# Optimization experiments

Hardware: AMD Instinct MI355X
Metric: run time of the kernel (lower is better)

Reference implementation:

```python
import jax, jax.numpy as jnp
import numpy as np

NUM_GRAPHS = 64

def setup_inputs() -> dict:
    key = jax.random.key(0)
    ks = jax.random.split(key, 10)
    N, E, D, V = 100000, 1600000, 64, 30
    node_types = jax.random.randint(ks[0], (N,), 0, V, dtype=jnp.int64 if jax.config.jax_enable_x64 else jnp.int32)
    edge_index = jax.random.randint(ks[1], (2, E), 0, N, dtype=jnp.int32)
    batch = jnp.sort(jax.random.randint(ks[2], (N,), 0, NUM_GRAPHS, dtype=jnp.int32))
    emb_table = jax.random.normal(ks[3], (V, D), dtype=jnp.float32)
    W1 = jax.random.normal(ks[4], (D, D), dtype=jnp.float32) / np.sqrt(D)
    W2 = jax.random.normal(ks[5], (D, D), dtype=jnp.float32) / np.sqrt(D)
    W3 = jax.random.normal(ks[6], (D, D), dtype=jnp.float32) / np.sqrt(D)
    b1 = jnp.zeros((D,), jnp.float32)
    b2 = jnp.zeros((D,), jnp.float32)
    b3 = jnp.zeros((D,), jnp.float32)
    return {"node_types": node_types, "edge_index": edge_index, "batch": batch,
            "emb_table": emb_table, "W1": W1, "b1": b1, "W2": W2, "b2": b2, "W3": W3, "b3": b3}

def _gcn_conv(x, W, b, row, col, norm, N):
    # x' = D^-1/2 (A+I) D^-1/2 (x @ W) + b   (PyG GCNConv semantics)
    h = x @ W
    msg = h[row] * norm[:, None]              # gather + edgewise scale
    out = jax.ops.segment_sum(msg, col, num_segments=N)  # scatter-add at targets
    return out + b

def reference(node_types, edge_index, batch, emb_table, W1, b1, W2, b2, W3, b3):
    N = node_types.shape[0]
    # add self-loops
    loops = jnp.arange(N, dtype=edge_index.dtype)
    row = jnp.concatenate([edge_index[0], loops])
    col = jnp.concatenate([edge_index[1], loops])
    # symmetric normalization on A + I
    deg = jax.ops.segment_sum(jnp.ones_like(col, dtype=jnp.float32), col, num_segments=N)
    dinv = jnp.where(deg > 0, jax.lax.rsqrt(deg), 0.0)
    norm = dinv[row] * dinv[col]
    x = emb_table[node_types]
    x = jax.nn.relu(_gcn_conv(x, W1, b1, row, col, norm, N))
    x = jax.nn.relu(_gcn_conv(x, W2, b2, row, col, norm, N))
    x = _gcn_conv(x, W3, b3, row, col, norm, N)
    # global mean pool over batch segments
    sums = jax.ops.segment_sum(x, batch, num_segments=NUM_GRAPHS)
    cnts = jax.ops.segment_sum(jnp.ones((N,), jnp.float32), batch, num_segments=NUM_GRAPHS)
    pooled = sums / jnp.maximum(cnts, 1.0)[:, None]
    # L2 normalize rows
    return pooled / jnp.linalg.norm(pooled, axis=1, keepdims=True)
```

## Files before the change

### kernel.cpp

```cpp
#include <hip/hip_runtime.h>
#include <hip/hip_fp16.h>

#define DD 64
#define NUM_GRAPHS 64
#define AGG_BLOCKS 2048
#define EB 512
#define BINW 256
#define MAXNB 512
#define EBIN_CAP 6144

typedef _Float16 h2_t __attribute__((ext_vector_type(2)));

__device__ __forceinline__ float fdot2u(unsigned a, unsigned b, float c) {
    return __builtin_amdgcn_fdot2(__builtin_bit_cast(h2_t, a),
                                  __builtin_bit_cast(h2_t, b), c, false);
}

__global__ __launch_bounds__(256) void k_hist(const int* __restrict__ col,
                                              int* __restrict__ H, int E, int NB, int CE) {
    __shared__ int h[MAXNB];
    int eb = blockIdx.x, t = threadIdx.x;
    for (int i = t; i < NB; i += 256) h[i] = 0;
    __syncthreads();
    int e0 = eb * CE, e1 = min(E, e0 + CE);
    for (int e = e0 + t; e < e1; e += 256) atomicAdd(&h[col[e] >> 8], 1);
    __syncthreads();
    for (int i = t; i < NB; i += 256) H[eb * NB + i] = h[i];
}

__global__ __launch_bounds__(256) void k_scanA(int* __restrict__ H,
                                               int* __restrict__ bintot, int NB) {
    __shared__ int s[256];
    int b = blockIdx.x, t = threadIdx.x;
    int i0 = (2 * t) * NB + b, i1 = (2 * t + 1) * NB + b;
    int v0 = H[i0], v1 = H[i1];
    int tot = v0 + v1;
    s[t] = tot;
    __syncthreads();
    for (int off = 1; off < 256; off <<= 1) {
        int tv = (t >= off) ? s[t - off] : 0;
        __syncthreads();
        s[t] += tv;
        __syncthreads();
    }
    int excl = s[t] - tot;
    H[i0] = excl;
    H[i1] = excl + v0;
    if (t == 255) bintot[b] = s[255];
}

__global__ void k_scanB(const int* __restrict__ bintot, int* __restrict__ binstart, int NB) {
    __shared__ int s[512];
    int t = threadIdx.x;
    int v = (t < NB) ? bintot[t] : 0;
    s[t] = v;
    __syncthreads();
    for (int off = 1; off < 512; off <<= 1) {
        int tv = (t >= off) ? s[t - off] : 0;
        __syncthreads();
        s[t] += tv;
        __syncthreads();
    }
    if (t < NB) binstart[t] = s[t] - v;
    if (t == 511) binstart[NB] = s[511];
}

__global__ __launch_bounds__(256) void k_scatbin(const int* __restrict__ row,
                                                 const int* __restrict__ col,
                                                 const int* __restrict__ H,
                                                 const int* __restrict__ binstart,
                                                 unsigned* __restrict__ binned,
                                                 int E, int NB, int CE) {
    __shared__ int off[MAXNB];
    int eb = blockIdx.x, t = threadIdx.x;
    for (int i = t; i < NB; i += 256) off[i] = binstart[i] + H[eb * NB + i];
    __syncthreads();
    int e0 = eb * CE, e1 = min(E, e0 + CE);
    for (int e = e0 + t; e < e1; e += 256) {
        int c = col[e], r = row[e];
        int slot = atomicAdd(&off[c >> 8], 1);
        binned[slot] = ((unsigned)(c & 255) << 24) | (unsigned)r;
    }
}

__global__ __launch_bounds__(256) void k_bincsr(const unsigned* __restrict__ binned,
                                                const int* __restrict__ binstart,
                                                const int* __restrict__ nt,
                                                int* __restrict__ srcidx,
                                                int* __restrict__ rowptr,
                                                float* __restrict__ dinv,
                                                int2* __restrict__ pk, int N, int NB) {
    __shared__ unsigned arr[EBIN_CAP];
    __shared__ int sorted_[EBIN_CAP];
    __shared__ int cnt[BINW];
    __shared__ int base[BINW];
    __shared__ int cursor[BINW];
    int b = blockIdx.x, t = threadIdx.x;
    int s0 = binstart[b], s1 = binstart[b + 1];
    int binsz = s1 - s0;
    if (binsz > EBIN_CAP) binsz = EBIN_CAP;
    cnt[t] = 0;
    for (int i = t; i < binsz; i += 256) arr[i] = binned[s0 + i];
    __syncthreads();
    for (int i = t; i < binsz; i += 256) atomicAdd(&cnt[arr[i] >> 24], 1);
    __syncthreads();
    int v = cnt[t];
    base[t] = v;
    __syncthreads();
    for (int off = 1; off < 256; off <<= 1) {
        int tv = (t >= off) ? base[t - off] : 0;
        __syncthreads();
        base[t] += tv;
        __syncthreads();
    }
    int excl = base[t] - v;
    __syncthreads();
    base[t] = excl;
    cursor[t] = excl;
    __syncthreads();
    for (int i = t; i < binsz; i += 256) {
        unsigned val = arr[i];
        int pos = atomicAdd(&cursor[val >> 24], 1);
        sorted_[pos] = (int)(val & 0xFFFFFF);
    }
    __syncthreads();
    for (int i = t; i < binsz; i += 256) srcidx[s0 + i] = sorted_[i];
    int node = b * BINW + t;
    if (node < N) {
        rowptr[node] = s0 + base[t];
        float di = rsqrtf((float)cnt[t] + 1.0f);
        dinv[node] = di;
        pk[node] = make_int2(nt[node], __float_as_int(di));
    }
    if (b == NB - 1 && t == 0) rowptr[N] = s1;
}

__global__ void k_buildepk(const int* __restrict__ srcidx, const int2* __restrict__ pk,
                           unsigned* __restrict__ epku, int E) {
    int i = blockIdx.x * blockDim.x + threadIdx.x;
    if (i >= E) return;
    int2 p = pk[srcidx[i]];
    epku[i] = ((unsigned)p.x << 16) |
              (unsigned)__half_as_ushort(__float2half(__int_as_float(p.y)));
}

__global__ void k_embW1(const float* __restrict__ emb, const float* __restrict__ W1,
                        float* __restrict__ embW1, int V) {
    __shared__ float er[DD];
    int v = blockIdx.x, j = threadIdx.x;
    er[j] = emb[v * DD + j];
    __syncthreads();
    float acc = 0.0f;
    #pragma unroll
    for (int d = 0; d < DD; ++d) acc += er[d] * W1[d * DD + j];
    embW1[v * DD + j] = acc;
}

__global__ void k_packW(const float* __restrict__ W, unsigned* __restrict__ Wpk) {
    int t = blockIdx.x * blockDim.x + threadIdx.x;
    if (t >= 32 * DD) return;
    int p = t >> 6, j = t & 63;
    __half2 h = __floats2half2_rn(W[(2 * p) * DD + j], W[(2 * p + 1) * DD + j]);
    Wpk[t] = __builtin_bit_cast(unsigned, h);
}

__device__ __forceinline__ float epi_dot_full(float v, const unsigned* Wc) {
    float vn = __shfl_xor(v, 1, 64);
    __half2 pr = __floats2half2_rn(v, vn);
    int vpk = __builtin_bit_cast(int, pr);
    float o0 = 0.f, o1 = 0.f, o2 = 0.f, o3 = 0.f;
    #pragma unroll
    for (int p = 0; p < 32; p += 4) {
        o0 = fdot2u((unsigned)__builtin_amdgcn_readlane(vpk, 2 * (p + 0)), Wc[p + 0], o0);
        o1 = fdot2u((unsigned)__builtin_amdgcn_readlane(vpk, 2 * (p + 1)), Wc[p + 1], o1);
        o2 = fdot2u((unsigned)__builtin_amdgcn_readlane(vpk, 2 * (p + 2)), Wc[p + 2], o2);
        o3 = fdot2u((unsigned)__builtin_amdgcn_readlane(vpk, 2 * (p + 3)), Wc[p + 3], o3);
    }
    return (o0 + o1) + (o2 + o3);
}

__device__ __forceinline__ float epi_dot_q(float4 v, const unsigned* Wc) {
    __half2 h0 = __floats2half2_rn(v.x, v.y);
    __half2 h1 = __floats2half2_rn(v.z, v.w);
    int vp0 = __builtin_bit_cast(int, h0);
    int vp1 = __builtin_bit_cast(int, h1);
    float o0 = 0.f, o1 = 0.f, o2 = 0.f, o3 = 0.f;
    #pragma unroll
    for (int p = 0; p < 32; p += 4) {
        o0 = fdot2u((unsigned)__builtin_amdgcn_readlane(vp0, (p + 0) >> 1), Wc[p + 0], o0);
        o1 = fdot2u((unsigned)__builtin_amdgcn_readlane(vp1, (p + 1) >> 1), Wc[p + 1], o1);
        o2 = fdot2u((unsigned)__builtin_amdgcn_readlane(vp0, (p + 2) >> 1), Wc[p + 2], o2);
        o3 = fdot2u((unsigned)__builtin_amdgcn_readlane(vp1, (p + 3) >> 1), Wc[p + 3], o3);
    }
    return (o0 + o1) + (o2 + o3);
}

__device__ __forceinline__ void acc_h4(float4& a, uint2 r) {
    float2 f0 = __half22float2(*(const __half2*)&r.x);
    float2 f1 = __half22float2(*(const __half2*)&r.y);
    a.x += f0.x; a.y += f0.y; a.z += f1.x; a.w += f1.y;
}

__device__ __forceinline__ float4 gather_sum_q(const int* __restrict__ srcidx,
                                               const __half* __restrict__ Hs,
                                               int s, int e, int g, int l) {
    float4 A = {0,0,0,0}, B = {0,0,0,0}, C = {0,0,0,0}, D = {0,0,0,0};
    int k = s;
    int kend = s + ((e - s) & ~15);
    if (k < kend) {
        uint2 r0 = *(const uint2*)(Hs + (long)srcidx[k + g] * DD + 4 * l);
        uint2 r1 = *(const uint2*)(Hs + (long)srcidx[k + 4 + g] * DD + 4 * l);
        uint2 r2 = *(const uint2*)(Hs + (long)srcidx[k + 8 + g] * DD + 4 * l);
        uint2 r3 = *(const uint2*)(Hs + (long)srcidx[k + 12 + g] * DD + 4 * l);
        k += 16;
        for (; k < kend; k += 16) {
            uint2 n0 = *(const uint2*)(Hs + (long)srcidx[k + g] * DD + 4 * l);
            uint2 n1 = *(const uint2*)(Hs + (long)srcidx[k + 4 + g] * DD + 4 * l);
            uint2 n2 = *(const uint2*)(Hs + (long)srcidx[k + 8 + g] * DD + 4 * l);
            uint2 n3 = *(const uint2*)(Hs + (long)srcidx[k + 12 + g] * DD + 4 * l);
            acc_h4(A, r0); acc_h4(B, r1); acc_h4(C, r2); acc_h4(D, r3);
            r0 = n0; r1 = n1; r2 = n2; r3 = n3;
        }
        acc_h4(A, r0); acc_h4(B, r1); acc_h4(C, r2); acc_h4(D, r3);
    }
    for (; k < e; k += 4) {
        if (k + g < e) {
            uint2 rr = *(const uint2*)(Hs + (long)srcidx[k + g] * DD + 4 * l);
            acc_h4(A, rr);
        }
    }
    A.x += B.x + C.x + D.x; A.y += B.y + C.y + D.y;
    A.z += B.z + C.z + D.z; A.w += B.w + C.w + D.w;
    A.x += __shfl_xor(A.x, 16, 64); A.x += __shfl_xor(A.x, 32, 64);
    A.y += __shfl_xor(A.y, 16, 64); A.y += __shfl_xor(A.y, 32, 64);
    A.z += __shfl_xor(A.z, 16, 64); A.z += __shfl_xor(A.z, 32, 64);
    A.w += __shfl_xor(A.w, 16, 64); A.w += __shfl_xor(A.w, 32, 64);
    return A;
}

__global__ __launch_bounds__(256, 4) void k_agg1_fused(const int* __restrict__ rowptr,
                                                    const unsigned* __restrict__ epku,
                                                    const int2* __restrict__ pk,
                                                    const float* __restrict__ embW1,
                                                    const float* __restrict__ b1,
                                                    const unsigned* __restrict__ W2pk,
                                                    __half* __restrict__ OUT, int N, int V) {
    __shared__ float ew[30 * DD];
    int tid = threadIdx.x;
    for (int k = tid; k < V * DD; k += 256) ew[k] = embW1[k];
    __syncthreads();
    int j = tid & 63;
    unsigned Wc[32];
    #pragma unroll
    for (int p = 0; p < 32; ++p) Wc[p] = W2pk[p * DD + j];
    float bj = b1[j];
    int wave0 = blockIdx.x * 4 + (tid >> 6);
    int wstride = gridDim.x * 4;
    for (int node = __builtin_amdgcn_readfirstlane(wave0); node < N;
         node += wstride) {
        int s = rowptr[node], e = rowptr[node + 1];
        float acc = 0.0f;
        int k = s;
        for (; k + 7 < e; k += 8) {
            unsigned u0 = epku[k],   u1 = epku[k+1], u2 = epku[k+2], u3 = epku[k+3];
            unsigned u4 = epku[k+4], u5 = epku[k+5], u6 = epku[k+6], u7 = epku[k+7];
            acc += ew[(u0 >> 16) * DD + j] * __half2float(__ushort_as_half((unsigned short)(u0 & 0xFFFF)))
                 + ew[(u1 >> 16) * DD + j] * __half2float(__ushort_as_half((unsigned short)(u1 & 0xFFFF)))
                 + ew[(u2 >> 16) * DD + j] * __half2float(__ushort_as_half((unsigned short)(u2 & 0xFFFF)))
                 + ew[(u3 >> 16) * DD + j] * __half2float(__ushort_as_half((unsigned short)(u3 & 0xFFFF)));
            acc += ew[(u4 >> 16) * DD + j] * __half2float(__ushort_as_half((unsigned short)(u4 & 0xFFFF)))
                 + ew[(u5 >> 16) * DD + j] * __half2float(__ushort_as_half((unsigned short)(u5 & 0xFFFF)))
                 + ew[(u6 >> 16) * DD + j] * __half2float(__ushort_as_half((unsigned short)(u6 & 0xFFFF)))
                 + ew[(u7 >> 16) * DD + j] * __half2float(__ushort_as_half((unsigned short)(u7 & 0xFFFF)));
        }
        for (; k < e; ++k) {
            unsigned u0 = epku[k];
            acc += ew[(u0 >> 16) * DD + j] * __half2float(__ushort_as_half((unsigned short)(u0 & 0xFFFF)));
        }
        int2 pc = pk[node];
        float dc = __int_as_float(pc.y);
        float v = (acc + ew[pc.x * DD + j] * dc) * dc + bj;
        v = fmaxf(v, 0.0f);
        OUT[(long)node * DD + j] = __float2half(epi_dot_full(v, Wc) * dc);
    }
}

__global__ __launch_bounds__(256, 4) void k_agg2_fused(const int* __restrict__ rowptr,
                                                    const int* __restrict__ srcidx,
                                                    const float* __restrict__ dinv,
                                                    const __half* __restrict__ Hs,
                                                    const float* __restrict__ b2,
                                                    const unsigned* __restrict__ W3pk,
                                                    __half* __restrict__ OUT, int N) {
    int tid = threadIdx.x;
    int lane = tid & 63;
    int g = lane >> 4, l = lane & 15;
    unsigned Wc[32];
    #pragma unroll
    for (int p = 0; p < 32; ++p) Wc[p] = W3pk[p * DD + lane];
    float4 bq = *(const float4*)(b2 + 4 * l);
    int wave0 = blockIdx.x * 4 + (tid >> 6);
    int wstride = gridDim.x * 4;
    for (int node = __builtin_amdgcn_readfirstlane(wave0); node < N;
         node += wstride) {
        int s = rowptr[node], e = rowptr[node + 1];
        float4 acc = gather_sum_q(srcidx, Hs, s, e, g, l);
        float dc = dinv[node];
        uint2 sr = *(const uint2*)(Hs + (long)node * DD + 4 * l);
        float2 s0 = __half22float2(*(const __half2*)&sr.x);
        float2 s1 = __half22float2(*(const __half2*)&sr.y);
        float4 v;
        v.x = fmaxf((acc.x + s0.x) * dc + bq.x, 0.f);
        v.y = fmaxf((acc.y + s0.y) * dc + bq.y, 0.f);
        v.z = fmaxf((acc.z + s1.x) * dc + bq.z, 0.f);
        v.w = fmaxf((acc.w + s1.y) * dc + bq.w, 0.f);
        OUT[(long)node * DD + lane] = __float2half(epi_dot_q(v, Wc) * dc);
    }
}

__global__ __launch_bounds__(256, 4) void k_agg3_pool(const int* __restrict__ rowptr,
                                                   const int* __restrict__ srcidx,
                                                   const float* __restrict__ dinv,
                                                   const __half* __restrict__ Hs,
                                                   const float* __restrict__ b3,
                                                   const int* __restrict__ batch,
                                                   float* __restrict__ pool,
                                                   int N, int chunk) {
    int tid = threadIdx.x;
    int lane = tid & 63;
    int g = lane >> 4, l = lane & 15;
    int w = __builtin_amdgcn_readfirstlane(blockIdx.x * 4 + (tid >> 6));
    int start = w * chunk;
    if (start >= N) return;
    int endn = min(N, start + chunk);
    float4 bq = *(const float4*)(b3 + 4 * l);
    int gcur = batch[start];
    float4 pacc = {0.f, 0.f, 0.f, 0.f};
    for (int node = start; node < endn; ++node) {
        int s = rowptr[node], e = rowptr[node + 1];
        float4 acc = gather_sum_q(srcidx, Hs, s, e, g, l);
        float dc = dinv[node];
        uint2 sr = *(const uint2*)(Hs + (long)node * DD + 4 * l);
        float2 s0 = __half22float2(*(const __half2*)&sr.x);
        float2 s1 = __half22float2(*(const __half2*)&sr.y);
        float4 v;
        v.x = (acc.x + s0.x) * dc + bq.x;
        v.y = (acc.y + s0.y) * dc + bq.y;
        v.z = (acc.z + s1.x) * dc + bq.z;
        v.w = (acc.w + s1.y) * dc + bq.w;
        int gb = batch[node];
        if (gb != gcur) {
            if (g == 0) {
                atomicAdd(&pool[gcur * DD + 4 * l + 0], pacc.x);
                atomicAdd(&pool[gcur * DD + 4 * l + 1], pacc.y);
                atomicAdd(&pool[gcur * DD + 4 * l + 2], pacc.z);
                atomicAdd(&pool[gcur * DD + 4 * l + 3], pacc.w);
            }
            gcur = gb;
            pacc = v;
        } else {
            pacc.x += v.x; pacc.y += v.y; pacc.z += v.z; pacc.w += v.w;
        }
    }
    if (g == 0) {
        atomicAdd(&pool[gcur * DD + 4 * l + 0], pacc.x);
        atomicAdd(&pool[gcur * DD + 4 * l + 1], pacc.y);
        atomicAdd(&pool[gcur * DD + 4 * l + 2], pacc.z);
        atomicAdd(&pool[gcur * DD + 4 * l + 3], pacc.w);
    }
}

__global__ void k_final(const float* __restrict__ pool, const int* __restrict__ batch,
                        float* __restrict__ out, int N) {
    int g = blockIdx.x, j = threadIdx.x;
    int lo = 0, hi = N;
    while (lo < hi) { int m = (lo + hi) >> 1; if (batch[m] < g) lo = m + 1; else hi = m; }
    int lo2 = lo; hi = N;
    while (lo2 < hi) { int m = (lo2 + hi) >> 1; if (batch[m] < g + 1) lo2 = m + 1; else hi = m; }
    float cnt = fmaxf((float)(lo2 - lo), 1.0f);
    float v = pool[g * DD + j] / cnt;
    float sq = v * v;
    #pragma unroll
    for (int off = 32; off > 0; off >>= 1) sq += __shfl_down(sq, off, 64);
    float nrm = __shfl(sq, 0, 64);
    out[g * DD + j] = v / sqrtf(nrm);
}

extern "C" void kernel_launch(void* const* d_in, const int* in_sizes, int n_in,
                              void* d_out, int out_size, void* d_ws, size_t ws_size,
                              hipStream_t stream) {
    const int*   node_types = (const int*)d_in[0];
    const int*   edge_index = (const int*)d_in[1];
    const int*   batch      = (const int*)d_in[2];
    const float* emb        = (const float*)d_in[3];
    const float* W1 = (const float*)d_in[4];
    const float* b1 = (const float*)d_in[5];
    const float* W2 = (const float*)d_in[6];
    const float* b2 = (const float*)d_in[7];
    const float* W3 = (const float*)d_in[8];
    const float* b3 = (const float*)d_in[9];
    const int N = in_sizes[0];
    const int E = in_sizes[1] / 2;
    const int V = in_sizes[3] / DD;
    const int* row = edge_index;
    const int* col = edge_index + E;
    const long ND = (long)N * DD;
    const int NB = (N + BINW - 1) / BINW;
    const int CE = (E + EB - 1) / EB;

    char* p = (char*)d_ws;
    __half*   hsA     = (__half*)p;       p += ND * sizeof(__half);
    __half*   hsB     = (__half*)p;       p += ND * sizeof(__half);
    int*      srcidx  = (int*)p;          p += (size_t)E * sizeof(int);
    unsigned* epku    = (unsigned*)p;     p += (size_t)E * sizeof(unsigned);
    unsigned* binned  = (unsigned*)p;     p += (size_t)E * sizeof(unsigned);
    int*      H       = (int*)p;          p += (size_t)EB * NB * sizeof(int);
    int*      bintot  = (int*)p;          p += (size_t)(NB + 4) * sizeof(int);
    int*      binstart= (int*)p;          p += (size_t)(NB + 4) * sizeof(int);
    float*    dinv    = (float*)p;        p += (size_t)N * sizeof(float);
    int2*     pk      = (int2*)p;         p += (size_t)N * sizeof(int2);
    int*      rowptr  = (int*)p;          p += (size_t)(N + 4) * sizeof(int);
    float*    pool    = (float*)p;        p += (size_t)NUM_GRAPHS * DD * sizeof(float);
    float*    embW1   = (float*)p;        p += (size_t)V * DD * sizeof(float);
    unsigned* W2pk    = (unsigned*)p;     p += 32 * DD * sizeof(unsigned);
    unsigned* W3pk    = (unsigned*)p;     p += 32 * DD * sizeof(unsigned);

    k_hist<<<EB, 256, 0, stream>>>(col, H, E, NB, CE);
    k_scanA<<<NB, 256, 0, stream>>>(H, bintot, NB);
    k_scanB<<<1, 512, 0, stream>>>(bintot, binstart, NB);
    k_scatbin<<<EB, 256, 0, stream>>>(row, col, H, binstart, binned, E, NB, CE);
    k_bincsr<<<NB, 256, 0, stream>>>(binned, binstart, node_types, srcidx, rowptr,
                                     dinv, pk, N, NB);
    k_buildepk<<<(E + 255) / 256, 256, 0, stream>>>(srcidx, pk, epku, E);

    k_embW1<<<V, DD, 0, stream>>>(emb, W1, embW1, V);
    k_packW<<<8, 256, 0, stream>>>(W2, W2pk);
    k_packW<<<8, 256, 0, stream>>>(W3, W3pk);

    k_agg1_fused<<<AGG_BLOCKS, 256, 0, stream>>>(rowptr, epku, pk, embW1, b1, W2pk,
                                                 hsA, N, V);
    k_agg2_fused<<<AGG_BLOCKS, 256, 0, stream>>>(rowptr, srcidx, dinv, hsA, b2, W3pk,
                                                 hsB, N);
    hipMemsetAsync(pool, 0, (size_t)(NUM_GRAPHS * DD) * sizeof(float), stream);
    const int totalWaves = AGG_BLOCKS * 4;
    const int chunk = (N + totalWaves - 1) / totalWaves;
    k_agg3_pool<<<AGG_BLOCKS, 256, 0, stream>>>(rowptr, srcidx, dinv, hsB, b3, batch,
                                                pool, N, chunk);
    k_final<<<NUM_GRAPHS, DD, 0, stream>>>(pool, batch, (float*)d_out, N);
}
```

Before: 306.0 us.

## Reorder matmuls after aggregation and defer W3 past mean pooling

Uses linearity to move each weight multiply to after neighbour aggregation instead of before it. Layer 1's epilogue no longer applies W2; layer 2 aggregates the raw activations, then applies W2, bias and ReLU. The W3 product and bias move out of the per-node loop into the final per-graph kernel, since the mean pool commutes with the linear map. This removes one per-node 64x64 matvec and a weight pack launch, but changes where fp16 rounding happens and adds a small matvec in k_final.

Result: faster. 295.6 us (-3.4%).

```diff
diff --git a/kernel.cpp b/kernel.cpp
--- a/kernel.cpp
+++ b/kernel.cpp
@@ -162,21 +162,6 @@
     int p = t >> 6, j = t & 63;
     __half2 h = __floats2half2_rn(W[(2 * p) * DD + j], W[(2 * p + 1) * DD + j]);
     Wpk[t] = __builtin_bit_cast(unsigned, h);
-}
-
-__device__ __forceinline__ float epi_dot_full(float v, const unsigned* Wc) {
-    float vn = __shfl_xor(v, 1, 64);
-    __half2 pr = __floats2half2_rn(v, vn);
-    int vpk = __builtin_bit_cast(int, pr);
-    float o0 = 0.f, o1 = 0.f, o2 = 0.f, o3 = 0.f;
-    #pragma unroll
-    for (int p = 0; p < 32; p += 4) {
-        o0 = fdot2u((unsigned)__builtin_amdgcn_readlane(vpk, 2 * (p + 0)), Wc[p + 0], o0);
-        o1 = fdot2u((unsigned)__builtin_amdgcn_readlane(vpk, 2 * (p + 1)), Wc[p + 1], o1);
-        o2 = fdot2u((unsigned)__builtin_amdgcn_readlane(vpk, 2 * (p + 2)), Wc[p + 2], o2);
-        o3 = fdot2u((unsigned)__builtin_amdgcn_readlane(vpk, 2 * (p + 3)), Wc[p + 3], o3);
-    }
-    return (o0 + o1) + (o2 + o3);
 }
 
 __device__ __forceinline__ float epi_dot_q(float4 v, const unsigned* Wc) {
@@ -243,16 +228,12 @@
                                                     const int2* __restrict__ pk,
                                                     const float* __restrict__ embW1,
                                                     const float* __restrict__ b1,
-                                                    const unsigned* __restrict__ W2pk,
                                                     __half* __restrict__ OUT, int N, int V) {
     __shared__ float ew[30 * DD];
     int tid = threadIdx.x;
     for (int k = tid; k < V * DD; k += 256) ew[k] = embW1[k];
     __syncthreads();
     int j = tid & 63;
-    unsigned Wc[32];
-    #pragma unroll
-    for (int p = 0; p < 32; ++p) Wc[p] = W2pk[p * DD + j];
     float bj = b1[j];
     int wave0 = blockIdx.x * 4 + (tid >> 6);
     int wstride = gridDim.x * 4;
@@ -281,7 +262,7 @@
         float dc = __int_as_float(pc.y);
         float v = (acc + ew[pc.x * DD + j] * dc) * dc + bj;
         v = fmaxf(v, 0.0f);
-        OUT[(long)node * DD + j] = __float2half(epi_dot_full(v, Wc) * dc);
+        OUT[(long)node * DD + j] = __float2half(v * dc);
     }
 }
 
@@ -290,15 +271,15 @@
                                                     const float* __restrict__ dinv,
                                                     const __half* __restrict__ Hs,
                                                     const float* __restrict__ b2,
-                                                    const unsigned* __restrict__ W3pk,
+                                                    const unsigned* __restrict__ W2pk,
                                                     __half* __restrict__ OUT, int N) {
     int tid = threadIdx.x;
     int lane = tid & 63;
     int g = lane >> 4, l = lane & 15;
     unsigned Wc[32];
     #pragma unroll
-    for (int p = 0; p < 32; ++p) Wc[p] = W3pk[p * DD + lane];
-    float4 bq = *(const float4*)(b2 + 4 * l);
+    for (int p = 0; p < 32; ++p) Wc[p] = W2pk[p * DD + lane];
+    float bl = b2[lane];
     int wave0 = blockIdx.x * 4 + (tid >> 6);
     int wstride = gridDim.x * 4;
     for (int node = __builtin_amdgcn_readfirstlane(wave0); node < N;
@@ -309,12 +290,14 @@
         uint2 sr = *(const uint2*)(Hs + (long)node * DD + 4 * l);
         float2 s0 = __half22float2(*(const __half2*)&sr.x);
         float2 s1 = __half22float2(*(const __half2*)&sr.y);
-        float4 v;
-        v.x = fmaxf((acc.x + s0.x) * dc + bq.x, 0.f);
-        v.y = fmaxf((acc.y + s0.y) * dc + bq.y, 0.f);
-        v.z = fmaxf((acc.z + s1.x) * dc + bq.z, 0.f);
-        v.w = fmaxf((acc.w + s1.y) * dc + bq.w, 0.f);
-        OUT[(long)node * DD + lane] = __float2half(epi_dot_q(v, Wc) * dc);
+        float4 t;
+        t.x = (acc.x + s0.x) * dc;
+        t.y = (acc.y + s0.y) * dc;
+        t.z = (acc.z + s1.x) * dc;
+        t.w = (acc.w + s1.y) * dc;
+        float u = epi_dot_q(t, Wc);
+        float v2 = fmaxf(u + bl, 0.f);
+        OUT[(long)node * DD + lane] = __float2half(v2 * dc);
     }
 }
 
@@ -322,7 +305,6 @@
                                                    const int* __restrict__ srcidx,
                                                    const float* __restrict__ dinv,
                                                    const __half* __restrict__ Hs,
-                                                   const float* __restrict__ b3,
                                                    const int* __restrict__ batch,
                                                    float* __restrict__ pool,
                                                    int N, int chunk) {
@@ -333,7 +315,6 @@
     int start = w * chunk;
     if (start >= N) return;
     int endn = min(N, start + chunk);
-    float4 bq = *(const float4*)(b3 + 4 * l);
     int gcur = batch[start];
     float4 pacc = {0.f, 0.f, 0.f, 0.f};
     for (int node = start; node < endn; ++node) {
@@ -344,10 +325,10 @@
         float2 s0 = __half22float2(*(const __half2*)&sr.x);
         float2 s1 = __half22float2(*(const __half2*)&sr.y);
         float4 v;
-        v.x = (acc.x + s0.x) * dc + bq.x;
-        v.y = (acc.y + s0.y) * dc + bq.y;
-        v.z = (acc.z + s1.x) * dc + bq.z;
-        v.w = (acc.w + s1.y) * dc + bq.w;
+        v.x = (acc.x + s0.x) * dc;
+        v.y = (acc.y + s0.y) * dc;
+        v.z = (acc.z + s1.x) * dc;
+        v.w = (acc.w + s1.y) * dc;
         int gb = batch[node];
         if (gb != gcur) {
             if (g == 0) {
@@ -371,14 +352,21 @@
 }
 
 __global__ void k_final(const float* __restrict__ pool, const int* __restrict__ batch,
+                        const float* __restrict__ W3, const float* __restrict__ b3,
                         float* __restrict__ out, int N) {
+    __shared__ float pr[DD];
     int g = blockIdx.x, j = threadIdx.x;
+    pr[j] = pool[g * DD + j];
+    __syncthreads();
     int lo = 0, hi = N;
     while (lo < hi) { int m = (lo + hi) >> 1; if (batch[m] < g) lo = m + 1; else hi = m; }
     int lo2 = lo; hi = N;
     while (lo2 < hi) { int m = (lo2 + hi) >> 1; if (batch[m] < g + 1) lo2 = m + 1; else hi = m; }
     float cnt = fmaxf((float)(lo2 - lo), 1.0f);
-    float v = pool[g * DD + j] / cnt;
+    float acc = 0.0f;
+    #pragma unroll
+    for (int d = 0; d < DD; ++d) acc += pr[d] * W3[d * DD + j];
+    float v = acc / cnt + b3[j];
     float sq = v * v;
     #pragma unroll
     for (int off = 32; off > 0; off >>= 1) sq += __shfl_down(sq, off, 64);
@@ -423,7 +411,6 @@
     float*    pool    = (float*)p;        p += (size_t)NUM_GRAPHS * DD * sizeof(float);
     float*    embW1   = (float*)p;        p += (size_t)V * DD * sizeof(float);
     unsigned* W2pk    = (unsigned*)p;     p += 32 * DD * sizeof(unsigned);
-    unsigned* W3pk    = (unsigned*)p;     p += 32 * DD * sizeof(unsigned);
 
     k_hist<<<EB, 256, 0, stream>>>(col, H, E, NB, CE);
     k_scanA<<<NB, 256, 0, stream>>>(H, bintot, NB);
@@ -435,16 +422,15 @@
 
     k_embW1<<<V, DD, 0, stream>>>(emb, W1, embW1, V);
     k_packW<<<8, 256, 0, stream>>>(W2, W2pk);
-    k_packW<<<8, 256, 0, stream>>>(W3, W3pk);
-
-    k_agg1_fused<<<AGG_BLOCKS, 256, 0, stream>>>(rowptr, epku, pk, embW1, b1, W2pk,
+
+    k_agg1_fused<<<AGG_BLOCKS, 256, 0, stream>>>(rowptr, epku, pk, embW1, b1,
                                                  hsA, N, V);
-    k_agg2_fused<<<AGG_BLOCKS, 256, 0, stream>>>(rowptr, srcidx, dinv, hsA, b2, W3pk,
+    k_agg2_fused<<<AGG_BLOCKS, 256, 0, stream>>>(rowptr, srcidx, dinv, hsA, b2, W2pk,
                                                  hsB, N);
     hipMemsetAsync(pool, 0, (size_t)(NUM_GRAPHS * DD) * sizeof(float), stream);
     const int totalWaves = AGG_BLOCKS * 4;
     const int chunk = (N + totalWaves - 1) / totalWaves;
-    k_agg3_pool<<<AGG_BLOCKS, 256, 0, stream>>>(rowptr, srcidx, dinv, hsB, b3, batch,
+    k_agg3_pool<<<AGG_BLOCKS, 256, 0, stream>>>(rowptr, srcidx, dinv, hsB, batch,
                                                 pool, N, chunk);
-    k_final<<<NUM_GRAPHS, DD, 0, stream>>>(pool, batch, (float*)d_out, N);
-}
+    k_final<<<NUM_GRAPHS, DD, 0, stream>>>(pool, batch, W3, b3, (float*)d_out, N);
+}
```
